# Performance work log

Hardware: AMD Instinct MI355X
Metric: run time of the kernel (lower is better)

The kernel has to match this reference:

```python
import jax, jax.numpy as jnp
from jax import lax
import numpy as np

B, C, S, H, DH, DV, DW = 16, 256, 64, 8, 32, 32, 32  # batch, channels, input_size, heads, d_h, d_v, d_w


def _dwconv(x, w, b):
    # depthwise 3x3 conv, stride 1, pad 1. w: [C,1,3,3]
    y = lax.conv_general_dilated(x, w, (1, 1), ((1, 1), (1, 1)),
                                 dimension_numbers=('NCHW', 'OIHW', 'NCHW'),
                                 feature_group_count=x.shape[1])
    return y + b[None, :, None, None]


def _linear(x, w, b):
    # torch Linear: w [out,in]
    return x @ w.T + b


def setup_inputs() -> dict:
    key = jax.random.key(0)
    ks = jax.random.split(key, 26)
    n = lambda k, shape, s=0.02: jax.random.normal(k, shape, jnp.float32) * s
    conv = lambda k: n(k, (C, 1, 3, 3), 0.1)
    return {
        'x': jax.random.normal(ks[0], (B, C, S, S), jnp.float32),
        'dw_qh_w': conv(ks[1]), 'dw_qh_b': n(ks[2], (C,)),
        'fc_qh_w': n(ks[3], (H * DH, C)), 'fc_qh_b': n(ks[4], (H * DH,)),
        'dw_kh_w': conv(ks[5]), 'dw_kh_b': n(ks[6], (C,)),
        'fc_kh_w': n(ks[7], (H * DH, C)), 'fc_kh_b': n(ks[8], (H * DH,)),
        'Bh': n(ks[9], (1, H, S, S)),
        'dw_v_w': conv(ks[10]), 'dw_v_b': n(ks[11], (C,)),
        'fc_v_w': n(ks[12], (H * DV, C)), 'fc_v_b': n(ks[13], (H * DV,)),
        'dw_qw_w': conv(ks[14]), 'dw_qw_b': n(ks[15], (C,)),
        'fc_qw_w': n(ks[16], (H * DW, C)), 'fc_qw_b': n(ks[17], (H * DW,)),
        'dw_kw_w': conv(ks[18]), 'dw_kw_b': n(ks[19], (C,)),
        'fc_kw_w': n(ks[20], (H * DW, C)), 'fc_kw_b': n(ks[21], (H * DW,)),
        'Bw': n(ks[22], (1, H, S, S)),
        'fc_o_w': n(ks[23], (C, H * DV)), 'fc_o_b': n(ks[24], (C,)),
    }


def reference(x, dw_qh_w, dw_qh_b, fc_qh_w, fc_qh_b,
              dw_kh_w, dw_kh_b, fc_kh_w, fc_kh_b, Bh,
              dw_v_w, dw_v_b, fc_v_w, fc_v_b,
              dw_qw_w, dw_qw_b, fc_qw_w, fc_qw_b,
              dw_kw_w, dw_kw_b, fc_kw_w, fc_kw_b, Bw,
              fc_o_w, fc_o_b):
    b, c, h, w = x.shape
    sh = DH ** -0.5
    sw = DW ** -0.5

    # height-axis queries/keys: dwconv -> adaptive avg pool over width -> linear
    qh = _dwconv(x, dw_qh_w, dw_qh_b).mean(axis=3).transpose(0, 2, 1)  # [b,h,c]
    qh = _linear(qh, fc_qh_w, fc_qh_b).reshape(b, h, H, DH).transpose(0, 2, 1, 3)  # [b,H,h,dh]
    kh = _dwconv(x, dw_kh_w, dw_kh_b).mean(axis=3).transpose(0, 2, 1)
    kh = _linear(kh, fc_kh_w, fc_kh_b).reshape(b, h, H, DH).transpose(0, 2, 1, 3)
    attn_h = jax.nn.softmax(jnp.einsum('bhid,bhjd->bhij', qh, kh) * sh + Bh, axis=-1)  # [b,H,h,h]

    # values over full HxW grid
    v = _dwconv(x, dw_v_w, dw_v_b).reshape(b, c, h * w).transpose(0, 2, 1)  # [b,hw,c]
    v = _linear(v, fc_v_w, fc_v_b).reshape(b, h, w, H, DV).transpose(0, 3, 1, 2, 4)  # [b,H,h,w,dv]
    v = v.reshape(b, H, h, w * DV)

    # width-axis queries/keys: dwconv -> adaptive avg pool over height -> linear
    qw = _dwconv(x, dw_qw_w, dw_qw_b).mean(axis=2).transpose(0, 2, 1)  # [b,w,c]
    qw = _linear(qw, fc_qw_w, fc_qw_b).reshape(b, w, H, DW).transpose(0, 2, 1, 3)  # [b,H,w,dw]
    kw = _dwconv(x, dw_kw_w, dw_kw_b).mean(axis=2).transpose(0, 2, 1)
    kw = _linear(kw, fc_kw_w, fc_kw_b).reshape(b, w, H, DW).transpose(0, 2, 1, 3)
    attn_w = jax.nn.softmax(jnp.einsum('bhid,bhjd->bhij', qw, kw) * sw + Bw, axis=-1)  # [b,H,w,w]

    # dual axial mixing: height attention, then width attention
    r = jnp.matmul(attn_h, v)                                # [b,H,h,w*dv]
    r = r.reshape(b, H, h, w, DV).transpose(0, 1, 2, 4, 3)    # [b,H,h,dv,w]
    r = r.reshape(b, H, h * DV, w)
    r = jnp.matmul(r, attn_w)                                # [b,H,h*dv,w]
    r = r.reshape(b, H, h, DV, w).transpose(0, 2, 4, 1, 3)    # [b,h,w,H,dv]
    r = r.reshape(b, h * w, H * DV)
    out = _linear(r, fc_o_w, fc_o_b).reshape(b, C, h, w)      # faithful to torch .view
    return out
```

## Files before the change

### kernel.cpp

```cpp
#include <hip/hip_runtime.h>
#include <hip/hip_bf16.h>

typedef float f4v __attribute__((ext_vector_type(4)));
typedef short s8v __attribute__((ext_vector_type(8)));
typedef unsigned short u8v __attribute__((ext_vector_type(8)));

__device__ __forceinline__ float bf2f(ushort u) {
  union { unsigned int i; float f; } c; c.i = ((unsigned int)u) << 16;
  return c.f;
}
__device__ __forceinline__ ushort f2bf(float f) {
  union { ushort s; __hip_bfloat16 h; } c; c.h = __float2bfloat16(f);
  return c.s;
}

__global__ __launch_bounds__(256) void k_prep(const float* __restrict__ w0,
                                              const float* __restrict__ w1,
                                              const float* __restrict__ w2,
                                              const float* __restrict__ w3,
                                              const float* __restrict__ wv,
                                              const float* __restrict__ wo,
                                              float* __restrict__ wt,
                                              ushort* __restrict__ wbf) {
  int bx = blockIdx.x;
  int tid = threadIdx.x;
  if (bx < 1024) {
    int mat = bx >> 8, o = bx & 255;
    const float* p = mat == 0 ? w0 : mat == 1 ? w1 : mat == 2 ? w2 : w3;
    wt[(size_t)mat * 65536 + (size_t)tid * 256 + o] = p[o * 256 + tid];
  } else {
    int idx = (bx - 1024) * 256 + tid;
    const float* src = (idx >> 16) ? wo : wv;
    wbf[idx] = f2bf(src[idx & 65535]);
  }
}

__global__ __launch_bounds__(256) void k_conv(
    const float* __restrict__ x,
    const float* __restrict__ wqh, const float* __restrict__ bqh,
    const float* __restrict__ wkh, const float* __restrict__ bkh,
    const float* __restrict__ wv,  const float* __restrict__ bv,
    const float* __restrict__ wqw, const float* __restrict__ bqw,
    const float* __restrict__ wkw, const float* __restrict__ bkw,
    ushort* __restrict__ convV,
    float* __restrict__ qhm, float* __restrict__ khm,
    float* __restrict__ qwm, float* __restrict__ kwm) {
  __shared__ float xs[68 * 68];
  __shared__ float wl[5][9];
  __shared__ float bl[5];

  int bx = blockIdx.x;
  int b = bx >> 8;
  int c = bx & 255;
  int tid = threadIdx.x;
  int lane = tid & 63, wave = tid >> 6;

  const float* xp = x + (size_t)(b * 256 + c) * 4096;
#pragma unroll
  for (int i = 0; i < 4; i++) {
    int flat = tid + i * 256;
    int r = flat >> 4, c4 = (flat & 15) * 4;
    float4 v = *(const float4*)(xp + r * 64 + c4);
    *(float4*)&xs[(r + 1) * 68 + 4 + c4] = v;
  }
  if (tid < 72) { xs[tid] = 0.f; xs[65 * 68 + tid] = 0.f; }
  if (tid >= 72 && tid < 200) {
    int t = tid - 72;
    int pr = (t & 63) + 1, side = t >> 6;
    xs[pr * 68 + (side ? 68 : 3)] = 0.f;
  }
  if (tid >= 200 && tid < 245) {
    int t = tid - 200;
    int cw = t / 9, wi = t % 9;
    const float* wp = cw == 0 ? wqh : cw == 1 ? wkh : cw == 2 ? wv
                    : cw == 3 ? wqw : wkw;
    wl[cw][wi] = wp[c * 9 + wi];
  } else if (tid >= 245 && tid < 250) {
    int cw = tid - 245;
    const float* bp = cw == 0 ? bqh : cw == 1 ? bkh : cw == 2 ? bv
                    : cw == 3 ? bqw : bkw;
    bl[cw] = bp[c];
  }
  __syncthreads();

  {
    int w = lane;
    int h0 = wave * 16;
    float v0 = wl[2][0], v1 = wl[2][1], v2 = wl[2][2];
    float v3 = wl[2][3], v4 = wl[2][4], v5 = wl[2][5];
    float v6 = wl[2][6], v7 = wl[2][7], v8 = wl[2][8];
    float bvv = bl[2];
    float a00 = xs[h0 * 68 + 3 + w], a01 = xs[h0 * 68 + 4 + w],
          a02 = xs[h0 * 68 + 5 + w];
    float a10 = xs[(h0 + 1) * 68 + 3 + w], a11 = xs[(h0 + 1) * 68 + 4 + w],
          a12 = xs[(h0 + 1) * 68 + 5 + w];
    ushort* cp = convV + (size_t)(b * 256 + c) * 4096 + h0 * 64 + w;
#pragma unroll
    for (int i = 0; i < 16; i++) {
      int pr = h0 + i + 2;
      float a20 = xs[pr * 68 + 3 + w];
      float a21 = xs[pr * 68 + 4 + w];
      float a22 = xs[pr * 68 + 5 + w];
      float acc = bvv;
      acc += a00 * v0 + a01 * v1 + a02 * v2;
      acc += a10 * v3 + a11 * v4 + a12 * v5;
      acc += a20 * v6 + a21 * v7 + a22 * v8;
      cp[i * 64] = f2bf(acc);
      a00 = a10; a01 = a11; a02 = a12;
      a10 = a20; a11 = a21; a12 = a22;
    }
  }

  if (wave == 0) {
    float rs = 0.f, e0 = 0.f, e1 = 0.f;
    const float* rowp = &xs[(lane + 1) * 68 + 4];
#pragma unroll
    for (int i = 0; i < 16; i++) {
      float4 v = *(const float4*)(rowp + i * 4);
      rs += (v.x + v.y) + (v.z + v.w);
      if (i == 0) e0 = v.x;
      if (i == 15) e1 = v.w;
    }
    float rsP = __shfl(rs, lane - 1, 64); rsP = (lane == 0) ? 0.f : rsP;
    float rsN = __shfl(rs, lane + 1, 64); rsN = (lane == 63) ? 0.f : rsN;
    float e0P = __shfl(e0, lane - 1, 64); e0P = (lane == 0) ? 0.f : e0P;
    float e0N = __shfl(e0, lane + 1, 64); e0N = (lane == 63) ? 0.f : e0N;
    float e1P = __shfl(e1, lane - 1, 64); e1P = (lane == 0) ? 0.f : e1P;
    float e1N = __shfl(e1, lane + 1, 64); e1N = (lane == 63) ? 0.f : e1N;
    float RS[3] = {rsP, rs, rsN};
    float E0[3] = {e0P, e0, e0N};
    float E1[3] = {e1P, e1, e1N};
    float vq = 0.f, vk = 0.f;
#pragma unroll
    for (int ky = 0; ky < 3; ky++) {
      vq += (wl[0][ky * 3] + wl[0][ky * 3 + 1] + wl[0][ky * 3 + 2]) * RS[ky]
            - wl[0][ky * 3] * E1[ky] - wl[0][ky * 3 + 2] * E0[ky];
      vk += (wl[1][ky * 3] + wl[1][ky * 3 + 1] + wl[1][ky * 3 + 2]) * RS[ky]
            - wl[1][ky * 3] * E1[ky] - wl[1][ky * 3 + 2] * E0[ky];
    }
    qhm[(size_t)(b * 256 + c) * 64 + lane] = vq * (1.f / 64.f) + bl[0];
    khm[(size_t)(b * 256 + c) * 64 + lane] = vk * (1.f / 64.f) + bl[1];
  } else if (wave == 1) {
    float cs = 0.f, f0 = 0.f, f1 = 0.f;
#pragma unroll
    for (int r = 0; r < 64; r++) {
      float v = xs[(r + 1) * 68 + 4 + lane];
      cs += v;
      if (r == 0) f0 = v;
      if (r == 63) f1 = v;
    }
    float csP = __shfl(cs, lane - 1, 64); csP = (lane == 0) ? 0.f : csP;
    float csN = __shfl(cs, lane + 1, 64); csN = (lane == 63) ? 0.f : csN;
    float f0P = __shfl(f0, lane - 1, 64); f0P = (lane == 0) ? 0.f : f0P;
    float f0N = __shfl(f0, lane + 1, 64); f0N = (lane == 63) ? 0.f : f0N;
    float f1P = __shfl(f1, lane - 1, 64); f1P = (lane == 0) ? 0.f : f1P;
    float f1N = __shfl(f1, lane + 1, 64); f1N = (lane == 63) ? 0.f : f1N;
    float CS[3] = {csP, cs, csN};
    float F0[3] = {f0P, f0, f0N};
    float F1[3] = {f1P, f1, f1N};
    float vq = 0.f, vk = 0.f;
#pragma unroll
    for (int kx = 0; kx < 3; kx++) {
      vq += (wl[3][kx] + wl[3][3 + kx] + wl[3][6 + kx]) * CS[kx]
            - wl[3][kx] * F1[kx] - wl[3][6 + kx] * F0[kx];
      vk += (wl[4][kx] + wl[4][3 + kx] + wl[4][6 + kx]) * CS[kx]
            - wl[4][kx] * F1[kx] - wl[4][6 + kx] * F0[kx];
    }
    qwm[(size_t)(b * 256 + c) * 64 + lane] = vq * (1.f / 64.f) + bl[3];
    kwm[(size_t)(b * 256 + c) * 64 + lane] = vk * (1.f / 64.f) + bl[4];
  }
}

template <int OUT_BF16, int AT>
__global__ __launch_bounds__(256) void k_mm(const ushort* __restrict__ A,
                                            const ushort* __restrict__ W,
                                            const float* __restrict__ bias,
                                            void* __restrict__ out) {
  __shared__ __align__(16) ushort As[128 * 40];
  __shared__ __align__(16) ushort Bs[128 * 40];

  int m0 = blockIdx.x * 128;
  int n0 = blockIdx.y * 128;
  int tid = threadIdx.x;
  int lane = tid & 63, wave = tid >> 6;
  int wm = (wave & 1) * 64, wn = (wave >> 1) * 64;
  int tm = lane & 15, quad = lane >> 4;

  const ushort* Abase;
  if (AT) {
    Abase = A + (size_t)(m0 >> 12) * (256 * 4096) + (m0 & 4095);
  } else {
    Abase = A + (size_t)m0 * 256;
  }

  f4v acc[4][4] = {};

  for (int kc = 0; kc < 256; kc += 32) {
    __syncthreads();
    if (AT) {
      int kr2 = (tid & 15) * 2, mg = tid >> 4;
      u8v v0 = *(const u8v*)&Abase[(size_t)(kc + kr2) * 4096 + mg * 8];
      u8v v1 = *(const u8v*)&Abase[(size_t)(kc + kr2 + 1) * 4096 + mg * 8];
#pragma unroll
      for (int j = 0; j < 8; j++) {
        ushort pr[2] = {v0[j], v1[j]};
        *(uint*)&As[(mg * 8 + j) * 40 + kr2] = *(uint*)pr;
      }
#pragma unroll
      for (int h = 0; h < 2; h++) {
        int ch = tid + h * 256;
        int mr = ch >> 2, k8 = (ch & 3) * 8;
        *(float4*)&Bs[mr * 40 + k8] =
            *(const float4*)&W[(size_t)(n0 + mr) * 256 + kc + k8];
      }
    } else {
#pragma unroll
      for (int h = 0; h < 2; h++) {
        int ch = tid + h * 256;
        int mr = ch >> 2, k8 = (ch & 3) * 8;
        *(float4*)&As[mr * 40 + k8] =
            *(const float4*)&Abase[(size_t)mr * 256 + kc + k8];
        *(float4*)&Bs[mr * 40 + k8] =
            *(const float4*)&W[(size_t)(n0 + mr) * 256 + kc + k8];
      }
    }
    __syncthreads();

    s8v a[4], bfr[4];
#pragma unroll
    for (int mi = 0; mi < 4; mi++)
      a[mi] = *(const s8v*)&As[(wm + mi * 16 + tm) * 40 + quad * 8];
#pragma unroll
    for (int ni = 0; ni < 4; ni++)
      bfr[ni] = *(const s8v*)&Bs[(wn + ni * 16 + tm) * 40 + quad * 8];
#pragma unroll
    for (int mi = 0; mi < 4; mi++)
#pragma unroll
      for (int ni = 0; ni < 4; ni++)
        acc[mi][ni] = __builtin_amdgcn_mfma_f32_16x16x32_bf16(
            a[mi], bfr[ni], acc[mi][ni], 0, 0, 0);
  }

#pragma unroll
  for (int mi = 0; mi < 4; mi++) {
#pragma unroll
    for (int ni = 0; ni < 4; ni++) {
      int col = n0 + wn + ni * 16 + tm;
      float bv = bias[col];
#pragma unroll
      for (int r = 0; r < 4; r++) {
        int row = m0 + wm + mi * 16 + quad * 4 + r;
        float v = acc[mi][ni][r] + bv;
        if (OUT_BF16)
          ((ushort*)out)[(size_t)row * 256 + col] = f2bf(v);
        else
          ((float*)out)[(size_t)row * 256 + col] = v;
      }
    }
  }
}

__global__ __launch_bounds__(256) void k_gemm4(
    const float* __restrict__ s0, const float* __restrict__ s1,
    const float* __restrict__ s2, const float* __restrict__ s3,
    const float* __restrict__ wt,
    const float* __restrict__ b0, const float* __restrict__ b1,
    const float* __restrict__ b2, const float* __restrict__ b3,
    float* __restrict__ d0, float* __restrict__ d1,
    float* __restrict__ d2, float* __restrict__ d3) {
  __shared__ __align__(16) float As[32 * 64];
  __shared__ __align__(16) float Ws[32 * 64];

  int z = blockIdx.z;
  const float* At = z == 0 ? s0 : z == 1 ? s1 : z == 2 ? s2 : s3;
  const float* Wt = wt + (size_t)z * 65536;
  const float* bias = z == 0 ? b0 : z == 1 ? b1 : z == 2 ? b2 : b3;
  float* Cout = z == 0 ? d0 : z == 1 ? d1 : z == 2 ? d2 : d3;

  int m0 = blockIdx.x * 64;
  int n0 = blockIdx.y * 64;
  int tid = threadIdx.x;
  const float* Ab = At + (size_t)(m0 >> 6) * 256 * 64;

  int tx = tid & 15, ty = tid >> 4;
  int lk = tid >> 6;
  int lm = tid & 63;
  float acc[4][4] = {};

  for (int kc = 0; kc < 256; kc += 32) {
    __syncthreads();
#pragma unroll
    for (int r = 0; r < 8; r++) {
      int kk = lk + r * 4;
      As[kk * 64 + lm] = Ab[(size_t)(kc + kk) * 64 + lm];
      Ws[kk * 64 + lm] = Wt[(kc + kk) * 256 + n0 + lm];
    }
    __syncthreads();
#pragma unroll
    for (int kk = 0; kk < 32; kk++) {
      float4 av = *(const float4*)&As[kk * 64 + ty * 4];
      float4 wv = *(const float4*)&Ws[kk * 64 + tx * 4];
      float a_[4] = {av.x, av.y, av.z, av.w};
      float w_[4] = {wv.x, wv.y, wv.z, wv.w};
#pragma unroll
      for (int ii = 0; ii < 4; ii++)
#pragma unroll
        for (int jj = 0; jj < 4; jj++) acc[ii][jj] += a_[ii] * w_[jj];
    }
  }

#pragma unroll
  for (int ii = 0; ii < 4; ii++) {
    int m = m0 + ty * 4 + ii;
#pragma unroll
    for (int jj = 0; jj < 4; jj++) {
      int n = n0 + tx * 4 + jj;
      Cout[(size_t)m * 256 + n] = acc[ii][jj] + bias[n];
    }
  }
}

__global__ __launch_bounds__(256) void k_attn(
    const float* __restrict__ qh, const float* __restrict__ kh,
    const float* __restrict__ Bh, float* __restrict__ ah,
    const float* __restrict__ qw, const float* __restrict__ kw,
    const float* __restrict__ Bw, float* __restrict__ aw, float scale) {
  __shared__ float qs[4][32];
  __shared__ float ks[64 * 33];

  int bx = blockIdx.x;
  int setw = bx >> 11;
  int rem = bx & 2047;
  int ig = rem & 15, hd = (rem >> 4) & 7, b = rem >> 7;
  int tid = threadIdx.x;
  int wave = tid >> 6, lane = tid & 63;
  int i = ig * 4 + wave;

  const float* q = setw ? qw : qh;
  const float* k = setw ? kw : kh;
  const float* Bb = setw ? Bw : Bh;
  float* attn = setw ? aw : ah;

  if (lane < 32) qs[wave][lane] = q[(size_t)(b * 64 + i) * 256 + hd * 32 + lane];
#pragma unroll
  for (int it = 0; it < 8; it++) {
    int f = tid + it * 256;
    int j = f >> 5, d = f & 31;
    ks[j * 33 + d] = k[(size_t)(b * 64 + j) * 256 + hd * 32 + d];
  }
  __syncthreads();

  int j = lane;
  float dot = 0.f;
#pragma unroll
  for (int d = 0; d < 32; d++) dot += qs[wave][d] * ks[j * 33 + d];
  float logit = dot * scale + Bb[(hd * 64 + i) * 64 + j];
  float mx = logit;
#pragma unroll
  for (int off = 32; off > 0; off >>= 1)
    mx = fmaxf(mx, __shfl_xor(mx, off, 64));
  float e = __expf(logit - mx);
  float sum = e;
#pragma unroll
  for (int off = 32; off > 0; off >>= 1) sum += __shfl_xor(sum, off, 64);
  attn[(size_t)((b * 8 + hd) * 64 + i) * 64 + j] = e / sum;
}

__global__ __launch_bounds__(256) void k_av(const float* __restrict__ attn,
                                            const ushort* __restrict__ vlin,
                                            ushort* __restrict__ r1) {
  __shared__ __align__(16) float As[64 * 65];
  __shared__ __align__(16) float Bs[64 * 64];

  int bx = blockIdx.x;
  int cc = bx & 31, hd = (bx >> 5) & 7, b = bx >> 8;
  int tid = threadIdx.x;
  int l = tid & 63, g = tid >> 6;

  const float* ap = attn + (size_t)(b * 8 + hd) * 4096;
#pragma unroll
  for (int r = 0; r < 16; r++) {
    int i = g + r * 4;
    As[l * 65 + i] = ap[i * 64 + l];
  }
  int colg0 = cc * 64;
#pragma unroll
  for (int r = 0; r < 8; r++) {
    int f = tid + r * 256;
    int j = f >> 5, p2 = f & 31;
    int colg = colg0 + p2 * 2;
    int w = colg >> 5, dv = colg & 31;
    uint u = *(const uint*)&vlin[(size_t)(b * 4096 + j * 64 + w) * 256 +
                                 hd * 32 + dv];
    Bs[j * 64 + p2 * 2] = bf2f((ushort)(u & 0xffff));
    Bs[j * 64 + p2 * 2 + 1] = bf2f((ushort)(u >> 16));
  }
  __syncthreads();

  int tx = tid & 15, ty = tid >> 4;
  float acc[4][4] = {};
  for (int j = 0; j < 64; j++) {
    float4 bv = *(const float4*)&Bs[j * 64 + tx * 4];
    float b_[4] = {bv.x, bv.y, bv.z, bv.w};
    float a_[4];
#pragma unroll
    for (int ii = 0; ii < 4; ii++) a_[ii] = As[j * 65 + ty * 4 + ii];
#pragma unroll
    for (int ii = 0; ii < 4; ii++)
#pragma unroll
      for (int jj = 0; jj < 4; jj++) acc[ii][jj] += a_[ii] * b_[jj];
  }

  ushort* rp = r1 + (size_t)(b * 8 + hd) * 64 * 2048;
#pragma unroll
  for (int ii = 0; ii < 4; ii++) {
    int row = ty * 4 + ii;
    ushort pk[4];
#pragma unroll
    for (int jj = 0; jj < 4; jj++) pk[jj] = f2bf(acc[ii][jj]);
    *(uint2*)&rp[(size_t)row * 2048 + colg0 + tx * 4] = *(uint2*)pk;
  }
}

__global__ __launch_bounds__(256) void k_rw(const ushort* __restrict__ r1,
                                            const float* __restrict__ attnw,
                                            ushort* __restrict__ yT) {
  __shared__ __align__(16) ushort As[8 * 2180];
  __shared__ __align__(16) ushort Wh[64 * 68];
  __shared__ __align__(16) ushort Wl[64 * 68];

  int bx = blockIdx.x;
  int ht = bx & 7, hd = (bx >> 3) & 7, b = bx >> 6;
  int tid = threadIdx.x;
  int lane = tid & 63, wave = tid >> 6;

  {
    int h = tid >> 5;
    int t = tid & 31;
    const ushort* rp =
        r1 + (size_t)((b * 8 + hd) * 64 + ht * 8 + h) * 2048;
#pragma unroll
    for (int i = 0; i < 4; i++) {
      int chunk = t + 32 * i;
      int w = (chunk >> 2) * 2;
      int dv0 = (chunk & 3) * 8;
      u8v v0 = *(const u8v*)&rp[w * 32 + dv0];
      u8v v1 = *(const u8v*)&rp[(w + 1) * 32 + dv0];
#pragma unroll
      for (int j = 0; j < 8; j++) {
        ushort pr[2] = {(ushort)v0[j], (ushort)v1[j]};
        *(uint*)&As[h * 2180 + (dv0 + j) * 68 + w] = *(uint*)pr;
      }
    }
  }
  {
    const float* ap = attnw + (size_t)(b * 8 + hd) * 4096;
#pragma unroll
    for (int p = 0; p < 4; p++) {
      int w = (tid >> 4) + p * 16;
      int wq = (tid & 15) * 4;
      float4 v = *(const float4*)&ap[w * 64 + wq];
      float f_[4] = {v.x, v.y, v.z, v.w};
#pragma unroll
      for (int j = 0; j < 4; j++) {
        ushort hi = f2bf(f_[j]);
        Wh[(wq + j) * 68 + w] = hi;
        Wl[(wq + j) * 68 + w] = f2bf(f_[j] - bf2f(hi));
      }
    }
  }
  __syncthreads();

  int tm = lane & 15, quad = lane >> 4;
  int h0 = wave * 2;
  f4v acc[4][4] = {};
#pragma unroll
  for (int kc = 0; kc < 64; kc += 32) {
    s8v a[4], bh[4], bl[4];
#pragma unroll
    for (int mi = 0; mi < 4; mi++) {
      int h = h0 + (mi >> 1);
      int dv = (mi & 1) * 16 + tm;
      int idx = h * 2180 + dv * 68 + kc + quad * 8;
      union { s8v v; unsigned long long u[2]; } t_;
      t_.u[0] = *(const unsigned long long*)&As[idx];
      t_.u[1] = *(const unsigned long long*)&As[idx + 4];
      a[mi] = t_.v;
    }
#pragma unroll
    for (int ni = 0; ni < 4; ni++) {
      int idx = (ni * 16 + tm) * 68 + kc + quad * 8;
      union { s8v v; unsigned long long u[2]; } th, tl;
      th.u[0] = *(const unsigned long long*)&Wh[idx];
      th.u[1] = *(const unsigned long long*)&Wh[idx + 4];
      tl.u[0] = *(const unsigned long long*)&Wl[idx];
      tl.u[1] = *(const unsigned long long*)&Wl[idx + 4];
      bh[ni] = th.v;
      bl[ni] = tl.v;
    }
#pragma unroll
    for (int mi = 0; mi < 4; mi++)
#pragma unroll
      for (int ni = 0; ni < 4; ni++) {
        acc[mi][ni] = __builtin_amdgcn_mfma_f32_16x16x32_bf16(
            a[mi], bh[ni], acc[mi][ni], 0, 0, 0);
        acc[mi][ni] = __builtin_amdgcn_mfma_f32_16x16x32_bf16(
            a[mi], bl[ni], acc[mi][ni], 0, 0, 0);
      }
  }

#pragma unroll
  for (int mi = 0; mi < 4; mi++) {
    int h = ht * 8 + h0 + (mi >> 1);
    int dv0 = (mi & 1) * 16 + quad * 4;
#pragma unroll
    for (int ni = 0; ni < 4; ni++) {
      int wp = ni * 16 + tm;
      ushort pk[4];
#pragma unroll
      for (int r = 0; r < 4; r++) pk[r] = f2bf(acc[mi][ni][r]);
      *(uint2*)&yT[(size_t)(b * 4096 + h * 64 + wp) * 256 + hd * 32 + dv0] =
          *(uint2*)pk;
    }
  }
}

extern "C" void kernel_launch(void* const* d_in, const int* in_sizes, int n_in,
                              void* d_out, int out_size, void* d_ws,
                              size_t ws_size, hipStream_t stream) {
  const float* x      = (const float*)d_in[0];
  const float* dwqh_w = (const float*)d_in[1];
  const float* dwqh_b = (const float*)d_in[2];
  const float* fcqh_w = (const float*)d_in[3];
  const float* fcqh_b = (const float*)d_in[4];
  const float* dwkh_w = (const float*)d_in[5];
  const float* dwkh_b = (const float*)d_in[6];
  const float* fckh_w = (const float*)d_in[7];
  const float* fckh_b = (const float*)d_in[8];
  const float* Bh     = (const float*)d_in[9];
  const float* dwv_w  = (const float*)d_in[10];
  const float* dwv_b  = (const float*)d_in[11];
  const float* fcv_w  = (const float*)d_in[12];
  const float* fcv_b  = (const float*)d_in[13];
  const float* dwqw_w = (const float*)d_in[14];
  const float* dwqw_b = (const float*)d_in[15];
  const float* fcqw_w = (const float*)d_in[16];
  const float* fcqw_b = (const float*)d_in[17];
  const float* dwkw_w = (const float*)d_in[18];
  const float* dwkw_b = (const float*)d_in[19];
  const float* fckw_w = (const float*)d_in[20];
  const float* fckw_b = (const float*)d_in[21];
  const float* Bw     = (const float*)d_in[22];
  const float* fco_w  = (const float*)d_in[23];
  const float* fco_b  = (const float*)d_in[24];

  char* base = (char*)d_ws;
  ushort* P1 = (ushort*)(base);
  ushort* P2 = (ushort*)(base + 33554432);
  ushort* P3 = (ushort*)(base + 67108864);
  float*  wt   = (float*)(base + 100663296);
  ushort* wv_bf = (ushort*)(base + 101711872);
  float* qhm = (float*)(base + 101974016);
  float* khm = qhm + 262144;
  float* qwm = khm + 262144;
  float* kwm = qwm + 262144;
  float* qhl = kwm + 262144;
  float* khl = qhl + 262144;
  float* qwl = khl + 262144;
  float* kwl = qwl + 262144;
  float* ah  = kwl + 262144;
  float* awt = ah + 524288;
  if (ws_size < 115000000ull) return;

  const float scale = 0.17677669529663687f;

  k_prep<<<1536, 256, 0, stream>>>(fcqh_w, fckh_w, fcqw_w, fckw_w, fcv_w,
                                   fco_w, wt, wv_bf);
  k_conv<<<4096, 256, 0, stream>>>(x, dwqh_w, dwqh_b, dwkh_w, dwkh_b, dwv_w,
                                   dwv_b, dwqw_w, dwqw_b, dwkw_w, dwkw_b, P1,
                                   qhm, khm, qwm, kwm);
  k_gemm4<<<dim3(16, 4, 4), 256, 0, stream>>>(qhm, khm, qwm, kwm, wt, fcqh_b,
                                              fckh_b, fcqw_b, fckw_b, qhl, khl,
                                              qwl, kwl);
  k_attn<<<4096, 256, 0, stream>>>(qhl, khl, Bh, ah, qwl, kwl, Bw, awt, scale);
  k_mm<1, 1><<<dim3(512, 2), 256, 0, stream>>>(P1, wv_bf, fcv_b, P3);
  k_av<<<4096, 256, 0, stream>>>(ah, P3, P1);
  k_rw<<<1024, 256, 0, stream>>>(P1, awt, P2);
  k_mm<0, 0><<<dim3(512, 2), 256, 0, stream>>>(P2, wv_bf + 65536, fco_b, d_out);
}
```

Before: 294.6 us.

## Use bf16 MFMA with split-precision attention in height-attention times V kernel

Rewrites the k_av kernel, which multiplies height attention by V, to use 16x16x32 bf16 MFMA instructions in place of the scalar fp32 FMA loop. The fp32 attention matrix is split into high and low bf16 parts to keep accuracy, while V is transposed into shared memory. Each block now covers 256 output columns instead of 64, so the launch shrinks to 1024 blocks and the attention tile is reloaded less often. The output is written as scattered 2-byte stores, which costs some write coalescing, and the larger shared-memory footprint may reduce occupancy.

```diff
diff --git a/kernel.cpp b/kernel.cpp
--- a/kernel.cpp
+++ b/kernel.cpp
@@ -369,56 +369,105 @@
 __global__ __launch_bounds__(256) void k_av(const float* __restrict__ attn,
                                             const ushort* __restrict__ vlin,
                                             ushort* __restrict__ r1) {
-  __shared__ __align__(16) float As[64 * 65];
-  __shared__ __align__(16) float Bs[64 * 64];
+  __shared__ __align__(16) ushort Ah[64 * 68];
+  __shared__ __align__(16) ushort Al[64 * 68];
+  __shared__ __align__(16) ushort Bt[256 * 68];
 
   int bx = blockIdx.x;
-  int cc = bx & 31, hd = (bx >> 5) & 7, b = bx >> 8;
+  int nt = bx & 7, hd = (bx >> 3) & 7, b = bx >> 6;
+  int n0 = nt * 256;
   int tid = threadIdx.x;
-  int l = tid & 63, g = tid >> 6;
+  int lane = tid & 63, wave = tid >> 6;
 
   const float* ap = attn + (size_t)(b * 8 + hd) * 4096;
-#pragma unroll
-  for (int r = 0; r < 16; r++) {
-    int i = g + r * 4;
-    As[l * 65 + i] = ap[i * 64 + l];
-  }
-  int colg0 = cc * 64;
-#pragma unroll
-  for (int r = 0; r < 8; r++) {
-    int f = tid + r * 256;
-    int j = f >> 5, p2 = f & 31;
-    int colg = colg0 + p2 * 2;
-    int w = colg >> 5, dv = colg & 31;
-    uint u = *(const uint*)&vlin[(size_t)(b * 4096 + j * 64 + w) * 256 +
-                                 hd * 32 + dv];
-    Bs[j * 64 + p2 * 2] = bf2f((ushort)(u & 0xffff));
-    Bs[j * 64 + p2 * 2 + 1] = bf2f((ushort)(u >> 16));
+  {
+    int i = tid >> 2;
+    int j0 = (tid & 3) * 16;
+#pragma unroll
+    for (int p = 0; p < 4; p++) {
+      float4 v = *(const float4*)&ap[i * 64 + j0 + p * 4];
+      float f_[4] = {v.x, v.y, v.z, v.w};
+      ushort ph[4], pl[4];
+#pragma unroll
+      for (int q = 0; q < 4; q++) {
+        ph[q] = f2bf(f_[q]);
+        pl[q] = f2bf(f_[q] - bf2f(ph[q]));
+      }
+      *(uint2*)&Ah[i * 68 + j0 + p * 4] = *(uint2*)ph;
+      *(uint2*)&Al[i * 68 + j0 + p * 4] = *(uint2*)pl;
+    }
+  }
+  {
+#pragma unroll
+    for (int p = 0; p < 4; p++) {
+      int task = tid + p * 256;
+      int jp = task & 31;
+      int cc = task >> 5;
+      int j = jp * 2;
+      int c = cc * 8;
+      int gcol = n0 + c;
+      int w = gcol >> 5, dv = gcol & 31;
+      const ushort* vp =
+          &vlin[(size_t)(b * 4096 + j * 64 + w) * 256 + hd * 32 + dv];
+      u8v v0 = *(const u8v*)vp;
+      u8v v1 = *(const u8v*)(vp + 64 * 256);
+#pragma unroll
+      for (int q = 0; q < 8; q++) {
+        ushort pr[2] = {(ushort)v0[q], (ushort)v1[q]};
+        *(uint*)&Bt[(c + q) * 68 + j] = *(uint*)pr;
+      }
+    }
   }
   __syncthreads();
 
-  int tx = tid & 15, ty = tid >> 4;
-  float acc[4][4] = {};
-  for (int j = 0; j < 64; j++) {
-    float4 bv = *(const float4*)&Bs[j * 64 + tx * 4];
-    float b_[4] = {bv.x, bv.y, bv.z, bv.w};
-    float a_[4];
-#pragma unroll
-    for (int ii = 0; ii < 4; ii++) a_[ii] = As[j * 65 + ty * 4 + ii];
-#pragma unroll
-    for (int ii = 0; ii < 4; ii++)
-#pragma unroll
-      for (int jj = 0; jj < 4; jj++) acc[ii][jj] += a_[ii] * b_[jj];
+  int tm = lane & 15, quad = lane >> 4;
+  int wn = wave * 64;
+  f4v acc[4][4] = {};
+#pragma unroll
+  for (int kc = 0; kc < 64; kc += 32) {
+    s8v ah_[4], al_[4], bb[4];
+#pragma unroll
+    for (int mi = 0; mi < 4; mi++) {
+      int idx = (mi * 16 + tm) * 68 + kc + quad * 8;
+      union { s8v v; unsigned long long u[2]; } th, tl;
+      th.u[0] = *(const unsigned long long*)&Ah[idx];
+      th.u[1] = *(const unsigned long long*)&Ah[idx + 4];
+      tl.u[0] = *(const unsigned long long*)&Al[idx];
+      tl.u[1] = *(const unsigned long long*)&Al[idx + 4];
+      ah_[mi] = th.v;
+      al_[mi] = tl.v;
+    }
+#pragma unroll
+    for (int ni = 0; ni < 4; ni++) {
+      int idx = (wn + ni * 16 + tm) * 68 + kc + quad * 8;
+      union { s8v v; unsigned long long u[2]; } tb;
+      tb.u[0] = *(const unsigned long long*)&Bt[idx];
+      tb.u[1] = *(const unsigned long long*)&Bt[idx + 4];
+      bb[ni] = tb.v;
+    }
+#pragma unroll
+    for (int mi = 0; mi < 4; mi++)
+#pragma unroll
+      for (int ni = 0; ni < 4; ni++) {
+        acc[mi][ni] = __builtin_amdgcn_mfma_f32_16x16x32_bf16(
+            ah_[mi], bb[ni], acc[mi][ni], 0, 0, 0);
+        acc[mi][ni] = __builtin_amdgcn_mfma_f32_16x16x32_bf16(
+            al_[mi], bb[ni], acc[mi][ni], 0, 0, 0);
+      }
   }
 
   ushort* rp = r1 + (size_t)(b * 8 + hd) * 64 * 2048;
 #pragma unroll
-  for (int ii = 0; ii < 4; ii++) {
-    int row = ty * 4 + ii;
-    ushort pk[4];
-#pragma unroll
-    for (int jj = 0; jj < 4; jj++) pk[jj] = f2bf(acc[ii][jj]);
-    *(uint2*)&rp[(size_t)row * 2048 + colg0 + tx * 4] = *(uint2*)pk;
+  for (int mi = 0; mi < 4; mi++) {
+#pragma unroll
+    for (int ni = 0; ni < 4; ni++) {
+      int col = n0 + wn + ni * 16 + tm;
+#pragma unroll
+      for (int r = 0; r < 4; r++) {
+        int row = mi * 16 + quad * 4 + r;
+        rp[(size_t)row * 2048 + col] = f2bf(acc[mi][ni][r]);
+      }
+    }
   }
 }
 
@@ -584,7 +633,7 @@
                                               qwl, kwl);
   k_attn<<<4096, 256, 0, stream>>>(qhl, khl, Bh, ah, qwl, kwl, Bw, awt, scale);
   k_mm<1, 1><<<dim3(512, 2), 256, 0, stream>>>(P1, wv_bf, fcv_b, P3);
-  k_av<<<4096, 256, 0, stream>>>(ah, P3, P1);
+  k_av<<<1024, 256, 0, stream>>>(ah, P3, P1);
   k_rw<<<1024, 256, 0, stream>>>(P1, awt, P2);
   k_mm<0, 0><<<dim3(512, 2), 256, 0, stream>>>(P2, wv_bf + 65536, fco_b, d_out);
 }
```

Result: faster. 280.9 us (-4.6%).
